# Performance work log

Hardware: AMD Instinct MI355X
Metric: run time of the kernel (lower is better)

Reference implementation:

```python
import jax, jax.numpy as jnp
import numpy as np

B, S, D, F, E = 4, 2048, 1024, 4096, 4


def setup_inputs() -> dict:
    key = jax.random.key(0)
    ks = jax.random.split(key, 8)
    sd = 1.0 / np.sqrt(D)  # torch Linear default init bound (fan_in = d_model)
    sf = 1.0 / np.sqrt(F)  # fan_in = d_ff
    return {
        "x": jax.random.normal(ks[0], (B, S, D), dtype=jnp.float32),
        # per-expert MLP params, stacked over expert dim E
        "W1": jax.random.uniform(ks[1], (E, D, F), jnp.float32, -sd, sd),
        "b1": jax.random.uniform(ks[2], (E, F), jnp.float32, -sd, sd),
        "W2": jax.random.uniform(ks[3], (E, F, D), jnp.float32, -sf, sf),
        "b2": jax.random.uniform(ks[4], (E, D), jnp.float32, -sf, sf),
        # uncertainty head: Linear(d_model, 1)
        "Wu": jax.random.uniform(ks[5], (D, 1), jnp.float32, -sd, sd),
        "bu": jax.random.uniform(ks[6], (1,), jnp.float32, -sd, sd),
    }


def reference(x, W1, b1, W2, b2, Wu, bu):
    # x: [B, S, D]
    n_exp = W1.shape[0]
    seq = x.shape[1]

    # uncertainty in (0,1), per token: sigmoid(Linear(x)).squeeze(-1)
    u = jax.nn.sigmoid(jnp.einsum("bsd,do->bso", x, Wu) + bu)[..., 0]  # [B,S]
    # variable number of experts per token in [1, E]
    k = jnp.clip(jnp.ceil(u * n_exp), 1, n_exp).astype(jnp.int32)  # [B,S]

    # dense all-expert MLP: every expert processes every token (faithful math;
    # original gathers only active tokens, but per-token result is identical)
    h = jax.nn.relu(jnp.einsum("bsd,edf->bsef", x, W1) + b1)  # [B,S,E,F]
    y = jnp.einsum("bsef,efd->bsed", h, W2) + b2               # [B,S,E,D]

    s_idx = jnp.arange(seq)
    out = jnp.zeros_like(x)
    for i in range(1, n_exp + 1):  # loop over small fixed expert count
        # expert assigned at pass i depends only on position: (s + i - 1) % E
        e_idx = (s_idx + i - 1) % n_exp  # [S]
        y_i = jnp.take_along_axis(y, e_idx[None, :, None, None], axis=2)[:, :, 0, :]  # [B,S,D]
        w = jnp.where(k >= i, u / i, 0.0)  # [B,S]
        out = out + w[..., None] * y_i
    return out
```

## Files before the change

kernel.cpp:

```cpp
#include <hip/hip_runtime.h>

#define DEV __device__ __forceinline__

typedef __attribute__((ext_vector_type(8))) short s16x8;
typedef __attribute__((ext_vector_type(4))) float f32x4;
typedef __attribute__((ext_vector_type(4))) unsigned short u16x4;

#define BTOK 8192
#define DD   1024
#define FF   4096
#define EE   4
#define BK   32

DEV unsigned short f2bf(float f) {
  unsigned int u = __float_as_uint(f);
  unsigned int r = (u + 0x7FFFu + ((u >> 16) & 1u)) >> 16;
  return (unsigned short)r;
}

DEV void gld_lds16(const void* g, void* l) {
  __builtin_amdgcn_global_load_lds(
      (const __attribute__((address_space(1))) unsigned int*)g,
      (__attribute__((address_space(3))) unsigned int*)l,
      16, 0, 0);
}

DEV void gemm_ring(const unsigned short* __restrict__ A,
                   const unsigned short* __restrict__ B,
                   int K, int tileM, int tileN,
                   unsigned short* As, unsigned short* Bs,
                   f32x4 (&acc)[8][4]) {
  const int t    = threadIdx.x;
  const int lane = t & 63;
  const int wid  = t >> 6;
  const int wr   = wid >> 2;
  const int wc   = wid & 3;
  const int m16  = lane & 15;
  const int quad = lane >> 4;

  const int rT   = t >> 2;
  const int sKey = (rT & 3) << 4;
  const int cSrc = ((((t & 3) << 4) ^ sKey) >> 1);
  const unsigned short* A0 = A + (size_t)(tileM + rT) * K + cSrc;
  const unsigned short* A1 = A + (size_t)(tileM + 128 + rT) * K + cSrc;
  const unsigned short* B0 = B + (size_t)(tileN + rT) * K + cSrc;
  const unsigned short* B1 = B + (size_t)(tileN + 128 + rT) * K + cSrc;
  const int ldsOff = t * 8;

  const int rKey  = (m16 & 3) << 4;
  const int cOffS = (((quad << 4) ^ rKey) >> 1);
  const int aBase = (wr * 128 + m16) * BK + cOffS;
  const int bBase = (wc * 64 + m16) * BK + cOffS;

  const int NT = K / BK;

#define STAGE(kt_)                                                            \
  {                                                                           \
    const int s_  = ((kt_) & 3) * 8192;                                       \
    const int ko_ = (kt_) * BK;                                               \
    gld_lds16(A0 + ko_, As + s_ + ldsOff);                                    \
    gld_lds16(A1 + ko_, As + s_ + 4096 + ldsOff);                             \
    gld_lds16(B0 + ko_, Bs + s_ + ldsOff);                                    \
    gld_lds16(B1 + ko_, Bs + s_ + 4096 + ldsOff);                             \
  }

  STAGE(0);
  STAGE(1);

  for (int kt = 0; kt < NT; ++kt) {
    if (kt + 2 < NT) {
      STAGE(kt + 2);
      asm volatile("s_waitcnt vmcnt(8)" ::: "memory");
    } else if (kt + 1 < NT) {
      asm volatile("s_waitcnt vmcnt(4)" ::: "memory");
    } else {
      asm volatile("s_waitcnt vmcnt(0)" ::: "memory");
    }
    __builtin_amdgcn_s_barrier();
    asm volatile("" ::: "memory");

    const int sb = (kt & 3) * 8192;

    s16x8 bF[4];
#pragma unroll
    for (int nt = 0; nt < 4; ++nt)
      bF[nt] = *(const s16x8*)(Bs + sb + bBase + nt * (16 * BK));

#pragma unroll
    for (int mp = 0; mp < 4; ++mp) {
      s16x8 a0 = *(const s16x8*)(As + sb + aBase + (2 * mp + 0) * (16 * BK));
      s16x8 a1 = *(const s16x8*)(As + sb + aBase + (2 * mp + 1) * (16 * BK));
      __builtin_amdgcn_s_setprio(1);
#pragma unroll
      for (int nt = 0; nt < 4; ++nt) {
        acc[2 * mp + 0][nt] = __builtin_amdgcn_mfma_f32_16x16x32_bf16(
            a0, bF[nt], acc[2 * mp + 0][nt], 0, 0, 0);
        acc[2 * mp + 1][nt] = __builtin_amdgcn_mfma_f32_16x16x32_bf16(
            a1, bF[nt], acc[2 * mp + 1][nt], 0, 0, 0);
      }
      __builtin_amdgcn_s_setprio(0);
    }
  }
#undef STAGE
}

__global__ __launch_bounds__(512, 2) void gemm1_kernel(
    const unsigned short* __restrict__ xb,
    const unsigned short* __restrict__ W1T,
    const float* __restrict__ b1,
    const float* __restrict__ c,
    unsigned short* __restrict__ h,
    int eBase) {
  __shared__ __attribute__((aligned(16))) unsigned short As[4 * 8192];
  __shared__ __attribute__((aligned(16))) unsigned short Bs[4 * 8192];

  const int bid = blockIdx.x;
  const int r   = bid & 7;
  const int pos = bid >> 3;
  const int rm  = r >> 1;
  const int rn  = r & 1;
  const int lm  = pos >> 3;
  const int ln  = pos & 7;
  const int tileM = (rm * 8 + lm) * 256;
  const int tileN = (rn * 8 + ln) * 256;

  const int e = eBase + blockIdx.z;

  f32x4 acc[8][4];
#pragma unroll
  for (int i = 0; i < 8; ++i)
#pragma unroll
    for (int j = 0; j < 4; ++j) acc[i][j] = f32x4{0.f, 0.f, 0.f, 0.f};

  gemm_ring(xb, W1T + (size_t)e * FF * DD, DD, tileM, tileN, As, Bs, acc);

  const int t = threadIdx.x;
  const int lane = t & 63, wid = t >> 6;
  const int wr = wid >> 2, wc = wid & 3;
  const int m16 = lane & 15, quad = lane >> 4;
  const float* b1e = b1 + e * FF;
  unsigned short* hs = h + (size_t)blockIdx.z * ((size_t)BTOK * FF);

#pragma unroll
  for (int mt = 0; mt < 8; ++mt) {
    const int row = tileM + wr * 128 + mt * 16 + quad * 4;
    const float cv0 = c[(row + 0) * EE + e];
    const float cv1 = c[(row + 1) * EE + e];
    const float cv2 = c[(row + 2) * EE + e];
    const float cv3 = c[(row + 3) * EE + e];
#pragma unroll
    for (int nt = 0; nt < 4; ++nt) {
      const int col = tileN + wc * 64 + nt * 16 + m16;
      const float bb = b1e[col];
      f32x4 v = acc[mt][nt];
      hs[(size_t)(row + 0) * FF + col] = f2bf(fmaxf(v[0] + bb, 0.f) * cv0);
      hs[(size_t)(row + 1) * FF + col] = f2bf(fmaxf(v[1] + bb, 0.f) * cv1);
      hs[(size_t)(row + 2) * FF + col] = f2bf(fmaxf(v[2] + bb, 0.f) * cv2);
      hs[(size_t)(row + 3) * FF + col] = f2bf(fmaxf(v[3] + bb, 0.f) * cv3);
    }
  }
}

__global__ __launch_bounds__(512, 2) void gemm2_kernel(
    const unsigned short* __restrict__ h,
    const unsigned short* __restrict__ W2T,
    float* __restrict__ out,
    int eBase) {
  __shared__ __attribute__((aligned(16))) unsigned short As[4 * 8192];
  __shared__ __attribute__((aligned(16))) unsigned short Bs[4 * 8192];

  const int bid = blockIdx.x;
  const int r   = bid & 7;
  const int pos = bid >> 3;
  const int tileM = (r * 4 + (pos >> 2)) * 256;
  const int tileN = (pos & 3) * 256;

  const int e = eBase + blockIdx.z;

  f32x4 acc[8][4];
#pragma unroll
  for (int i = 0; i < 8; ++i)
#pragma unroll
    for (int j = 0; j < 4; ++j) acc[i][j] = f32x4{0.f, 0.f, 0.f, 0.f};

  gemm_ring(h + (size_t)blockIdx.z * BTOK * FF,
            W2T + (size_t)e * DD * FF,
            FF, tileM, tileN, As, Bs, acc);

  const int t = threadIdx.x;
  const int lane = t & 63, wid = t >> 6;
  const int wr = wid >> 2, wc = wid & 3;
  const int m16 = lane & 15, quad = lane >> 4;

#pragma unroll
  for (int mt = 0; mt < 8; ++mt) {
    const int row = tileM + wr * 128 + mt * 16 + quad * 4;
#pragma unroll
    for (int nt = 0; nt < 4; ++nt) {
      const int col = tileN + wc * 64 + nt * 16 + m16;
      f32x4 v = acc[mt][nt];
      atomicAdd(&out[(size_t)(row + 0) * DD + col], v[0]);
      atomicAdd(&out[(size_t)(row + 1) * DD + col], v[1]);
      atomicAdd(&out[(size_t)(row + 2) * DD + col], v[2]);
      atomicAdd(&out[(size_t)(row + 3) * DD + col], v[3]);
    }
  }
}

__global__ __launch_bounds__(256) void u_kernel(
    const float* __restrict__ x,
    const float* __restrict__ Wu,
    const float* __restrict__ bu,
    const float* __restrict__ b2,
    float* __restrict__ c,
    float* __restrict__ out) {
  const int tok = blockIdx.x;
  const int tid = threadIdx.x;
  const float* xr = x + (size_t)tok * DD;

  f32x4 xv = ((const f32x4*)xr)[tid];
  f32x4 wv = ((const f32x4*)Wu)[tid];
  float s = xv[0] * wv[0] + xv[1] * wv[1] + xv[2] * wv[2] + xv[3] * wv[3];
#pragma unroll
  for (int off = 32; off > 0; off >>= 1) s += __shfl_down(s, off);

  __shared__ float red[4];
  __shared__ float cL[4];
  if ((tid & 63) == 0) red[tid >> 6] = s;
  __syncthreads();
  if (tid == 0) {
    float dot = red[0] + red[1] + red[2] + red[3] + bu[0];
    float u = 1.f / (1.f + expf(-dot));
    float kf = ceilf(u * 4.f);
    kf = fminf(fmaxf(kf, 1.f), 4.f);
    int k = (int)kf;
    int s4 = tok & 3;
#pragma unroll
    for (int e = 0; e < EE; ++e) {
      int i = ((e - s4) & 3) + 1;
      float ce = (i <= k) ? (u / (float)i) : 0.f;
      cL[e] = ce;
      c[tok * EE + e] = ce;
    }
  }
  __syncthreads();
  const float c0 = cL[0], c1 = cL[1], c2 = cL[2], c3 = cL[3];
#pragma unroll
  for (int d = tid; d < DD; d += 256)
    out[(size_t)tok * DD + d] =
        c0 * b2[d] + c1 * b2[DD + d] + c2 * b2[2 * DD + d] + c3 * b2[3 * DD + d];
}

__global__ __launch_bounds__(256) void cvt_kernel(const float* __restrict__ in,
                                                  unsigned short* __restrict__ ob,
                                                  int n4) {
  int i = blockIdx.x * 256 + threadIdx.x;
  if (i >= n4) return;
  f32x4 a = ((const f32x4*)in)[i];
  u16x4 o = {f2bf(a[0]), f2bf(a[1]), f2bf(a[2]), f2bf(a[3])};
  ((u16x4*)ob)[i] = o;
}

__global__ __launch_bounds__(256) void tpose_kernel(const float* __restrict__ src,
                                                    unsigned short* __restrict__ dst,
                                                    int R, int C) {
  __shared__ float tile[32][33];
  const int e = blockIdx.z;
  const int r0 = blockIdx.y * 32, c0 = blockIdx.x * 32;
  const int tx = threadIdx.x & 31, ty = threadIdx.x >> 5;
  const float* s = src + (size_t)e * R * C;
  unsigned short* d = dst + (size_t)e * C * R;
#pragma unroll
  for (int j = 0; j < 32; j += 8)
    tile[ty + j][tx] = s[(size_t)(r0 + ty + j) * C + (c0 + tx)];
  __syncthreads();
#pragma unroll
  for (int j = 0; j < 32; j += 8)
    d[(size_t)(c0 + ty + j) * R + (r0 + tx)] = f2bf(tile[tx][ty + j]);
}

extern "C" void kernel_launch(void* const* d_in, const int* in_sizes, int n_in,
                              void* d_out, int out_size, void* d_ws, size_t ws_size,
                              hipStream_t stream) {
  const float* x  = (const float*)d_in[0];
  const float* W1 = (const float*)d_in[1];
  const float* b1 = (const float*)d_in[2];
  const float* W2 = (const float*)d_in[3];
  const float* b2 = (const float*)d_in[4];
  const float* Wu = (const float*)d_in[5];
  const float* bu = (const float*)d_in[6];
  float* out = (float*)d_out;

  char* w = (char*)d_ws;
  unsigned short* xb  = (unsigned short*)w;  w += (size_t)BTOK * DD * 2;
  unsigned short* W1T = (unsigned short*)w;  w += (size_t)EE * DD * FF * 2;
  unsigned short* W2T = (unsigned short*)w;  w += (size_t)EE * FF * DD * 2;
  float* c = (float*)w;                      w += (size_t)BTOK * EE * 4;
  unsigned short* h = (unsigned short*)w;
  size_t used = (size_t)(w - (char*)d_ws);
  size_t hOne = (size_t)BTOK * FF * 2;

  size_t avail = (ws_size > used) ? (ws_size - used) : 0;
  int hSlots = (int)(avail / hOne);
  if (hSlots < 1) hSlots = 1;
  if (hSlots > EE) hSlots = EE;

  cvt_kernel<<<(BTOK * DD / 4 + 255) / 256, 256, 0, stream>>>(x, xb, BTOK * DD / 4);
  tpose_kernel<<<dim3(FF / 32, DD / 32, EE), 256, 0, stream>>>(W1, W1T, DD, FF);
  tpose_kernel<<<dim3(DD / 32, FF / 32, EE), 256, 0, stream>>>(W2, W2T, FF, DD);
  u_kernel<<<BTOK, 256, 0, stream>>>(x, Wu, bu, b2, c, out);

  for (int g = 0; g < EE; g += hSlots) {
    int cnt = (EE - g < hSlots) ? (EE - g) : hSlots;
    gemm1_kernel<<<dim3(512, 1, cnt), 512, 0, stream>>>(xb, W1T, b1, c, h, g);
    gemm2_kernel<<<dim3(128, 1, cnt), 512, 0, stream>>>(h, W2T, out, g);
  }
}
```

Before: 884.9 us.

## Double K-tile depth, use 2-stage LDS buffer and 4-phase quadrant MFMA schedule

The GEMM main loop now uses BK=64 with a 2-deep LDS double buffer instead of a 4-deep BK=32 ring, with a new XOR swizzle. Each K-tile's compute is split into four quadrant phases, each separated by a barrier and a sched_barrier, which reloads A/B fragments per quadrant. The aim is to halve per-K-step barrier and issue overhead and keep register pressure low while staying inside the same 128KB of LDS. In exchange there are more barriers per tile and only one stage of prefetch lookahead.

```diff
diff --git a/kernel.cpp b/kernel.cpp
--- a/kernel.cpp
+++ b/kernel.cpp
@@ -10,7 +10,7 @@
 #define DD   1024
 #define FF   4096
 #define EE   4
-#define BK   32
+#define BK   64
 
 DEV unsigned short f2bf(float f) {
   unsigned int u = __float_as_uint(f);
@@ -28,7 +28,7 @@
 DEV void gemm_ring(const unsigned short* __restrict__ A,
                    const unsigned short* __restrict__ B,
                    int K, int tileM, int tileN,
-                   unsigned short* As, unsigned short* Bs,
+                   unsigned short* Ls,
                    f32x4 (&acc)[8][4]) {
   const int t    = threadIdx.x;
   const int lane = t & 63;
@@ -38,69 +38,96 @@
   const int m16  = lane & 15;
   const int quad = lane >> 4;
 
-  const int rT   = t >> 2;
-  const int sKey = (rT & 3) << 4;
-  const int cSrc = ((((t & 3) << 4) ^ sKey) >> 1);
-  const unsigned short* A0 = A + (size_t)(tileM + rT) * K + cSrc;
-  const unsigned short* A1 = A + (size_t)(tileM + 128 + rT) * K + cSrc;
-  const unsigned short* B0 = B + (size_t)(tileN + rT) * K + cSrc;
-  const unsigned short* B1 = B + (size_t)(tileN + 128 + rT) * K + cSrc;
-  const int ldsOff = t * 8;
-
-  const int rKey  = (m16 & 3) << 4;
-  const int cOffS = (((quad << 4) ^ rKey) >> 1);
-  const int aBase = (wr * 128 + m16) * BK + cOffS;
-  const int bBase = (wc * 64 + m16) * BK + cOffS;
+  const int rT   = t >> 3;
+  const int cSrc = (((t & 7) ^ (rT & 7)) << 3);
+  const unsigned short* Ag = A + (size_t)(tileM + rT) * K + cSrc;
+  const unsigned short* Bg = B + (size_t)(tileN + rT) * K + cSrc;
+  const int dOff = t * 8;
+
+  const int sw0 = (((0 * 64 + quad * 16) ^ ((m16 & 7) << 4)) >> 1);
+  const int sw1 = (((1 * 64 + quad * 16) ^ ((m16 & 7) << 4)) >> 1);
 
   const int NT = K / BK;
 
 #define STAGE(kt_)                                                            \
   {                                                                           \
-    const int s_  = ((kt_) & 3) * 8192;                                       \
-    const int ko_ = (kt_) * BK;                                               \
-    gld_lds16(A0 + ko_, As + s_ + ldsOff);                                    \
-    gld_lds16(A1 + ko_, As + s_ + 4096 + ldsOff);                             \
-    gld_lds16(B0 + ko_, Bs + s_ + ldsOff);                                    \
-    gld_lds16(B1 + ko_, Bs + s_ + 4096 + ldsOff);                             \
-  }
+    const int bq_ = ((kt_) & 1) << 15;                  \
+    const size_t ko_ = (size_t)(kt_) * BK;                                    \
+    _Pragma("unroll") for (int j = 0; j < 4; ++j) {                           \
+      gld_lds16(Ag + (size_t)j * 64 * K + ko_, Ls + bq_ + j * 4096 + dOff);   \
+      gld_lds16(Bg + (size_t)j * 64 * K + ko_,                                \
+                Ls + bq_ + 16384 + j * 4096 + dOff);                          \
+    }                                                                         \
+  }
+
+#define LOAD_A(mh_)                                                           \
+  {                                                                           \
+    _Pragma("unroll") for (int ms = 0; ms < 4; ++ms) {                        \
+      const int rb_ = Ab + ((wr * 128 + (mh_)*64 + ms * 16 + m16) << 6);      \
+      aF[ms * 2 + 0] = *(const s16x8*)(Ls + rb_ + sw0);                       \
+      aF[ms * 2 + 1] = *(const s16x8*)(Ls + rb_ + sw1);                       \
+    }                                                                         \
+  }
+
+#define LOAD_B(nh_)                                                           \
+  {                                                                           \
+    _Pragma("unroll") for (int ns = 0; ns < 2; ++ns) {                        \
+      const int rb_ = Bb + ((wc * 64 + (nh_)*32 + ns * 16 + m16) << 6);       \
+      bF[ns * 2 + 0] = *(const s16x8*)(Ls + rb_ + sw0);                       \
+      bF[ns * 2 + 1] = *(const s16x8*)(Ls + rb_ + sw1);                       \
+    }                                                                         \
+  }
+
+#define MFMA_Q(mh_, nh_)                                                      \
+  {                                                                           \
+    __builtin_amdgcn_s_setprio(1);                                            \
+    _Pragma("unroll") for (int ms = 0; ms < 4; ++ms)                          \
+        _Pragma("unroll") for (int ns = 0; ns < 2; ++ns) {                    \
+      acc[(mh_)*4 + ms][(nh_)*2 + ns] =                                       \
+          __builtin_amdgcn_mfma_f32_16x16x32_bf16(                            \
+              aF[ms * 2 + 0], bF[ns * 2 + 0],                                 \
+              acc[(mh_)*4 + ms][(nh_)*2 + ns], 0, 0, 0);                      \
+      acc[(mh_)*4 + ms][(nh_)*2 + ns] =                                       \
+          __builtin_amdgcn_mfma_f32_16x16x32_bf16(                            \
+              aF[ms * 2 + 1], bF[ns * 2 + 1],                                 \
+              acc[(mh_)*4 + ms][(nh_)*2 + ns], 0, 0, 0);                      \
+    }                                                                         \
+    __builtin_amdgcn_s_setprio(0);                                            \
+  }
+
+#define PHASE_BAR()                                                           \
+  __builtin_amdgcn_s_barrier();                                               \
+  asm volatile("" ::: "memory");                                              \
+  __builtin_amdgcn_sched_barrier(0)
 
   STAGE(0);
-  STAGE(1);
 
   for (int kt = 0; kt < NT; ++kt) {
-    if (kt + 2 < NT) {
-      STAGE(kt + 2);
+    if (kt + 1 < NT) {
+      STAGE(kt + 1);
       asm volatile("s_waitcnt vmcnt(8)" ::: "memory");
-    } else if (kt + 1 < NT) {
-      asm volatile("s_waitcnt vmcnt(4)" ::: "memory");
     } else {
       asm volatile("s_waitcnt vmcnt(0)" ::: "memory");
     }
-    __builtin_amdgcn_s_barrier();
-    asm volatile("" ::: "memory");
-
-    const int sb = (kt & 3) * 8192;
-
-    s16x8 bF[4];
-#pragma unroll
-    for (int nt = 0; nt < 4; ++nt)
-      bF[nt] = *(const s16x8*)(Bs + sb + bBase + nt * (16 * BK));
-
-#pragma unroll
-    for (int mp = 0; mp < 4; ++mp) {
-      s16x8 a0 = *(const s16x8*)(As + sb + aBase + (2 * mp + 0) * (16 * BK));
-      s16x8 a1 = *(const s16x8*)(As + sb + aBase + (2 * mp + 1) * (16 * BK));
-      __builtin_amdgcn_s_setprio(1);
-#pragma unroll
-      for (int nt = 0; nt < 4; ++nt) {
-        acc[2 * mp + 0][nt] = __builtin_amdgcn_mfma_f32_16x16x32_bf16(
-            a0, bF[nt], acc[2 * mp + 0][nt], 0, 0, 0);
-        acc[2 * mp + 1][nt] = __builtin_amdgcn_mfma_f32_16x16x32_bf16(
-            a1, bF[nt], acc[2 * mp + 1][nt], 0, 0, 0);
-      }
-      __builtin_amdgcn_s_setprio(0);
-    }
-  }
+    PHASE_BAR();
+
+    const int Ab = (kt & 1) << 15;
+    const int Bb = Ab + 16384;
+    s16x8 aF[8], bF[4];
+
+    LOAD_A(0); LOAD_B(0); MFMA_Q(0, 0);
+    PHASE_BAR();
+    LOAD_B(1); MFMA_Q(0, 1);
+    PHASE_BAR();
+    LOAD_A(1); MFMA_Q(1, 1);
+    PHASE_BAR();
+    LOAD_B(0); MFMA_Q(1, 0);
+    PHASE_BAR();
+  }
+#undef PHASE_BAR
+#undef MFMA_Q
+#undef LOAD_B
+#undef LOAD_A
 #undef STAGE
 }
 
@@ -111,18 +138,15 @@
     const float* __restrict__ c,
     unsigned short* __restrict__ h,
     int eBase) {
-  __shared__ __attribute__((aligned(16))) unsigned short As[4 * 8192];
-  __shared__ __attribute__((aligned(16))) unsigned short Bs[4 * 8192];
+  __shared__ __attribute__((aligned(16))) unsigned short Ls[65536];
 
   const int bid = blockIdx.x;
   const int r   = bid & 7;
   const int pos = bid >> 3;
   const int rm  = r >> 1;
   const int rn  = r & 1;
-  const int lm  = pos >> 3;
-  const int ln  = pos & 7;
-  const int tileM = (rm * 8 + lm) * 256;
-  const int tileN = (rn * 8 + ln) * 256;
+  const int tileM = (rm * 8 + (pos >> 3)) * 256;
+  const int tileN = (rn * 8 + (pos & 7)) * 256;
 
   const int e = eBase + blockIdx.z;
 
@@ -132,7 +156,7 @@
 #pragma unroll
     for (int j = 0; j < 4; ++j) acc[i][j] = f32x4{0.f, 0.f, 0.f, 0.f};
 
-  gemm_ring(xb, W1T + (size_t)e * FF * DD, DD, tileM, tileN, As, Bs, acc);
+  gemm_ring(xb, W1T + (size_t)e * FF * DD, DD, tileM, tileN, Ls, acc);
 
   const int t = threadIdx.x;
   const int lane = t & 63, wid = t >> 6;
@@ -166,8 +190,7 @@
     const unsigned short* __restrict__ W2T,
     float* __restrict__ out,
     int eBase) {
-  __shared__ __attribute__((aligned(16))) unsigned short As[4 * 8192];
-  __shared__ __attribute__((aligned(16))) unsigned short Bs[4 * 8192];
+  __shared__ __attribute__((aligned(16))) unsigned short Ls[65536];
 
   const int bid = blockIdx.x;
   const int r   = bid & 7;
@@ -185,7 +208,7 @@
 
   gemm_ring(h + (size_t)blockIdx.z * BTOK * FF,
             W2T + (size_t)e * DD * FF,
-            FF, tileM, tileN, As, Bs, acc);
+            FF, tileM, tileN, Ls, acc);
 
   const int t = threadIdx.x;
   const int lane = t & 63, wid = t >> 6;
```

Result: no change. 868.0 us (-1.9%).
